# Kernel tuning notes

Hardware: AMD Instinct MI355X
Metric: run time of the kernel (lower is better)

The kernel has to match this reference:

```python
import jax, jax.numpy as jnp
import numpy as np

B_SCENES = 2; K = 5; C = 128; H = 64; W = 64
D_INNER = C; D_STATE = 16; DT_RANK = 8
C_TUKEY = 0.3; ALPHA = 2.0; BETA = 0.4; GAMMA = 0.8


def affine_grid(theta, Ho, Wo):
    # torch F.affine_grid, align_corners=False (pixel centers)
    xs = (jnp.arange(Wo, dtype=jnp.float32) + 0.5) * (2.0 / Wo) - 1.0
    ys = (jnp.arange(Ho, dtype=jnp.float32) + 0.5) * (2.0 / Ho) - 1.0
    gx, gy = jnp.meshgrid(xs, ys)
    base = jnp.stack([gx, gy, jnp.ones_like(gx)], axis=-1)  # (H,W,3)
    return jnp.einsum('nij,hwj->nhwi', theta, base)  # (N,H,W,2)


def grid_sample(src, grid):
    # bilinear, zero padding, align_corners=False; src (N,C,H,W), grid (N,H,W,2)
    N, Cc, Hs, Ws = src.shape
    ix = ((grid[..., 0] + 1.0) * Ws - 1.0) * 0.5
    iy = ((grid[..., 1] + 1.0) * Hs - 1.0) * 0.5
    x0 = jnp.floor(ix); y0 = jnp.floor(iy)
    def tap(xf, yf):
        v = ((xf >= 0) & (xf <= Ws - 1) & (yf >= 0) & (yf <= Hs - 1)).astype(src.dtype)
        xc = jnp.clip(xf, 0, Ws - 1).astype(jnp.int32)
        yc = jnp.clip(yf, 0, Hs - 1).astype(jnp.int32)
        vals = jax.vmap(lambda s, y, x: s[:, y, x])(src, yc, xc)  # (N,C,H,W)
        return vals * v[:, None]
    wx1 = (ix - x0)[:, None]; wy1 = (iy - y0)[:, None]
    wx0 = 1.0 - wx1; wy0 = 1.0 - wy1
    return (tap(x0, y0) * wx0 * wy0 + tap(x0 + 1.0, y0) * wx1 * wy0
            + tap(x0, y0 + 1.0) * wx0 * wy1 + tap(x0 + 1.0, y0 + 1.0) * wx1 * wy1)


def ss2d(tokens, in_proj_w, conv_w, conv_b, x_proj_w, dt_w, dt_b, A_logs, Ds, ln_g, ln_b, out_proj_w):
    # tokens (C, Hs, Ws) channel-first; VMamba-style v05_noz core, d_inner=C
    xin = jnp.einsum('chw,dc->dhw', tokens, in_proj_w)
    xc = jax.lax.conv_general_dilated(xin[None], conv_w, (1, 1), [(1, 1), (1, 1)],
                                      dimension_numbers=('NCHW', 'OIHW', 'NCHW'),
                                      feature_group_count=D_INNER)[0] + conv_b[:, None, None]
    xa = jax.nn.silu(xc)
    d, Hs, Ws = xa.shape
    L = Hs * Ws
    x_hw = xa.reshape(d, L)
    x_wh = jnp.swapaxes(xa, 1, 2).reshape(d, L)
    xs = jnp.stack([x_hw, x_wh, x_hw[:, ::-1], x_wh[:, ::-1]], axis=0)  # (4,d,L)
    x_dbl = jnp.einsum('kdl,kcd->kcl', xs, x_proj_w)
    dt = x_dbl[:, :DT_RANK]
    Bm = x_dbl[:, DT_RANK:DT_RANK + D_STATE]
    Cm = x_dbl[:, DT_RANK + D_STATE:]
    dts = jax.nn.softplus(jnp.einsum('kdr,krl->kdl', dt_w, dt) + dt_b[..., None])
    A = -jnp.exp(A_logs)  # (4,d,n)
    seq = (jnp.moveaxis(xs, -1, 0), jnp.moveaxis(dts, -1, 0),
           jnp.moveaxis(Bm, -1, 0), jnp.moveaxis(Cm, -1, 0))
    def step(h, inp):
        xt, dtt, Bt, Ct = inp
        h = h * jnp.exp(dtt[..., None] * A) + (dtt * xt)[..., None] * Bt[:, None, :]
        return h, jnp.einsum('kdn,kn->kd', h, Ct)
    h0 = jnp.zeros((4, d, D_STATE), tokens.dtype)
    _, ys = jax.lax.scan(jax.checkpoint(step), h0, seq)  # ys (L,4,d)
    ys = jnp.moveaxis(ys, 0, -1) + Ds[..., None] * xs  # (4,d,L)
    untr = lambda y: jnp.swapaxes(y.reshape(d, Ws, Hs), 1, 2).reshape(d, L)
    y = ys[0] + untr(ys[1]) + ys[2][:, ::-1] + untr(ys[3][:, ::-1])
    yt = y.T  # (L,d)
    mu = yt.mean(-1, keepdims=True)
    var = ((yt - mu) ** 2).mean(-1, keepdims=True)
    yn = (yt - mu) * jax.lax.rsqrt(var + 1e-5) * ln_g + ln_b
    out = yn @ out_proj_w.T  # (L,C)
    return jnp.moveaxis(out.reshape(Hs, Ws, -1), -1, 0)  # (C,Hs,Ws)


def forward(x, nam, in_proj_w, conv_w, conv_b, x_proj_w, dt_w, dt_b, A_logs, Ds, ln_g, ln_b, out_proj_w):
    xg = x.reshape(B_SCENES, K, C, H, W)  # record_len is constant K
    t_rows = nam[:, 0]  # ego row i=0 of t_matrix: (B,K,2,3)
    def scene(xb, t_row):
        warped = grid_sample(xb, affine_grid(t_row, H, W))  # (K,C,H,W)
        ego = warped[0]
        # per-pixel cosine sim across channels (F.normalize(dim=0) on (C,HW) views)
        en = ego / jnp.maximum(jnp.sqrt((ego ** 2).sum(0, keepdims=True)), 1e-6)
        nb = warped / jnp.maximum(jnp.sqrt((warped ** 2).sum(1, keepdims=True)), 1e-6)
        sims = jnp.clip((en[None] * nb).sum(1), -1.0, 1.0)  # (K,H,W)
        r = jnp.maximum(1.0 - sims, 0.0)
        xr = jnp.maximum(r / C_TUKEY, 0.0)
        w_pix = jnp.maximum(jnp.maximum(1.0 - xr * xr, 0.0) ** 2, 1e-6)[:, None]  # (K,1,H,W)
        tx = t_row[:, 0, 2]; ty = t_row[:, 1, 2]
        yaw = jnp.abs(jnp.arctan2(t_row[:, 0, 1], t_row[:, 0, 0]))
        g = jax.nn.sigmoid(ALPHA - BETA * jnp.sqrt(tx ** 2 + ty ** 2) - GAMMA * yaw)  # (K,)
        logit = jnp.log(w_pix + 1e-8) + jnp.log(g + 1e-8)[:, None, None, None]
        alpha = jax.nn.softmax(logit, axis=0)  # softmax over K per pixel
        weighted = warped * alpha
        tokens = jnp.swapaxes(weighted.reshape(K, C, H * W), 0, 1)  # (C,K,HW)
        out = ss2d(tokens, in_proj_w, conv_w, conv_b, x_proj_w, dt_w, dt_b,
                   A_logs, Ds, ln_g, ln_b, out_proj_w)  # (C,K,HW)
        return jnp.swapaxes(out, 0, 1).reshape(K, C, W, H)[0]  # (C,W,H) as in original view
    return jax.vmap(scene)(xg, t_rows)


def setup_inputs() -> dict:
    key = jax.random.key(0)
    ks = jax.random.split(key, 10)
    x = jax.random.normal(ks[0], (B_SCENES * K, C, H, W), jnp.float32)
    record_len = jnp.full((B_SCENES,), K, dtype=jnp.int32)
    eye = jnp.broadcast_to(jnp.array([[1.0, 0.0, 0.0], [0.0, 1.0, 0.0]], jnp.float32),
                           (B_SCENES, K, K, 2, 3))
    nam = eye + 0.05 * jax.random.normal(ks[1], (B_SCENES, K, K, 2, 3), jnp.float32)
    in_proj_w = 0.05 * jax.random.normal(ks[2], (D_INNER, C), jnp.float32)
    conv_w = 0.1 * jax.random.normal(ks[3], (D_INNER, 1, 3, 3), jnp.float32)
    conv_b = jnp.zeros((D_INNER,), jnp.float32)
    x_proj_w = 0.05 * jax.random.normal(ks[4], (4, DT_RANK + 2 * D_STATE, D_INNER), jnp.float32)
    dt_w = 0.1 * jax.random.normal(ks[5], (4, D_INNER, DT_RANK), jnp.float32)
    dt_b = -4.6 + 0.5 * jax.random.normal(ks[6], (4, D_INNER), jnp.float32)
    A_logs = jnp.broadcast_to(jnp.log(jnp.arange(1, D_STATE + 1, dtype=jnp.float32)),
                              (4, D_INNER, D_STATE)) + jnp.zeros((4, D_INNER, D_STATE), jnp.float32)
    Ds = jnp.ones((4, D_INNER), jnp.float32)
    ln_g = jnp.ones((D_INNER,), jnp.float32)
    ln_b = jnp.zeros((D_INNER,), jnp.float32)
    out_proj_w = 0.05 * jax.random.normal(ks[7], (C, D_INNER), jnp.float32)
    return {"x": x, "record_len": record_len, "normalized_affine_matrix": nam,
            "in_proj_w": in_proj_w, "conv_w": conv_w, "conv_b": conv_b,
            "x_proj_w": x_proj_w, "dt_w": dt_w, "dt_b": dt_b, "A_logs": A_logs,
            "Ds": Ds, "ln_g": ln_g, "ln_b": ln_b, "out_proj_w": out_proj_w}


def reference(x, record_len, normalized_affine_matrix, in_proj_w, conv_w, conv_b,
              x_proj_w, dt_w, dt_b, A_logs, Ds, ln_g, ln_b, out_proj_w):
    # record_len is a constant (= K per scene) and only determines the static grouping
    return forward(x, normalized_affine_matrix, in_proj_w, conv_w, conv_b,
                   x_proj_w, dt_w, dt_b, A_logs, Ds, ln_g, ln_b, out_proj_w)
```

## Files before the change

kernel.cpp:

```cpp
#include <hip/hip_runtime.h>
#include <math.h>

#define B_S   2
#define PIX   4096
#define LL    20480
#define NS    16
#define RR    8
#define NCHK  512
#define LC    40
#define SUBS  10
#define NSUB  4
#define NGRP  32
#define GCH   16
#define K0CH  104

typedef float v2f __attribute__((ext_vector_type(2)));
typedef float v4f __attribute__((ext_vector_type(4)));

__device__ __forceinline__ v2f pk_mul(v2f a, v2f b) {
  v2f d;
  asm("v_pk_mul_f32 %0, %1, %2" : "=v"(d) : "v"(a), "v"(b));
  return d;
}
#define PK_FMA_ACC(a, b, c) asm("v_pk_fma_f32 %0, %1, %2, %0" : "+v"(a) : "v"(b), "v"(c))
#define PK_DECAY(h, e, m) asm("v_pk_fma_f32 %0, %0, %1, %2" : "+v"(h) : "v"(e), "v"(m))

template<int K>
__device__ __forceinline__ int zmapT(int l) {
  if (K == 0) return l;
  if (K == 1) return ((l % 5) << 12) + l / 5;
  if (K == 2) return 20479 - l;
  int lr = 20479 - l;
  return ((lr % 5) << 12) + lr / 5;
}

__global__ __launch_bounds__(256)
void k_warp(const float* __restrict__ x, const float* __restrict__ nam,
            float* __restrict__ warped) {
  __shared__ float wL[4][64];
  __shared__ int   iL[4][64];
  int blk = blockIdx.x;
  int bk = blk >> 11;
  int rem = blk & 2047;
  int ct = rem >> 6, pt = rem & 63;
  int p0 = pt * 64;
  int t = threadIdx.x;
  int pl = t & 63, cg = t >> 6;
  if (t < 64) {
    int b = bk / 5, k = bk - b * 5;
    const float* th = nam + (size_t)(b * 25 + k) * 6;
    int p = p0 + t;
    float gx = ((p & 63) + 0.5f) * 0.03125f - 1.0f;
    float gy = ((p >> 6) + 0.5f) * 0.03125f - 1.0f;
    float grx = th[0] * gx + th[1] * gy + th[2];
    float gry = th[3] * gx + th[4] * gy + th[5];
    float ix = ((grx + 1.0f) * 64.0f - 1.0f) * 0.5f;
    float iy = ((gry + 1.0f) * 64.0f - 1.0f) * 0.5f;
    float x0 = floorf(ix), y0 = floorf(iy);
    float fx = ix - x0, fy = iy - y0;
    float vx0 = (x0 >= 0.0f && x0 <= 63.0f) ? 1.0f : 0.0f;
    float vx1 = (x0 >= -1.0f && x0 <= 62.0f) ? 1.0f : 0.0f;
    float vy0 = (y0 >= 0.0f && y0 <= 63.0f) ? 1.0f : 0.0f;
    float vy1 = (y0 >= -1.0f && y0 <= 62.0f) ? 1.0f : 0.0f;
    int xi0 = (int)fminf(fmaxf(x0, 0.0f), 63.0f);
    int yi0 = (int)fminf(fmaxf(y0, 0.0f), 63.0f);
    int xi1 = (int)fminf(fmaxf(x0 + 1.0f, 0.0f), 63.0f);
    int yi1 = (int)fminf(fmaxf(y0 + 1.0f, 0.0f), 63.0f);
    wL[0][t] = (1.0f - fx) * (1.0f - fy) * vx0 * vy0;
    wL[1][t] = fx * (1.0f - fy) * vx1 * vy0;
    wL[2][t] = (1.0f - fx) * fy * vx0 * vy1;
    wL[3][t] = fx * fy * vx1 * vy1;
    iL[0][t] = yi0 * 64 + xi0;
    iL[1][t] = yi0 * 64 + xi1;
    iL[2][t] = yi1 * 64 + xi0;
    iL[3][t] = yi1 * 64 + xi1;
  }
  __syncthreads();
  int c = ct * 4 + cg;
  const float* src = x + (size_t)(bk * 128 + c) * PIX;
  float acc = wL[0][pl] * src[iL[0][pl]]
            + wL[1][pl] * src[iL[1][pl]]
            + wL[2][pl] * src[iL[2][pl]]
            + wL[3][pl] * src[iL[3][pl]];
  warped[((size_t)(bk * 128 + c)) * PIX + p0 + pl] = acc;
}

__global__ __launch_bounds__(512)
void k_alpha(const float* __restrict__ warped, const float* __restrict__ nam,
             float* __restrict__ alpha) {
  __shared__ float part[8][64][9];
  int blk = blockIdx.x;
  int b = blk >> 6;
  int p0 = (blk & 63) << 6;
  int wv = threadIdx.x >> 6, lane = threadIdx.x & 63;
  int p = p0 + lane;
  const float* wb = warped + (size_t)b * 5 * 128 * PIX + p;
  float dot[5] = {0,0,0,0,0}, ssq[5] = {0,0,0,0,0};
  int c0 = wv * 16;
  for (int c = c0; c < c0 + 16; ++c) {
    float w0 = wb[(size_t)c * PIX];
    ssq[0] += w0 * w0;
    #pragma unroll
    for (int k = 1; k < 5; ++k) {
      float wk = wb[((size_t)k * 128 + c) * PIX];
      dot[k] += w0 * wk;
      ssq[k] += wk * wk;
    }
  }
  part[wv][lane][0] = ssq[0];
  #pragma unroll
  for (int k = 1; k < 5; ++k) {
    part[wv][lane][k] = dot[k];
    part[wv][lane][4 + k] = ssq[k];
  }
  __syncthreads();
  if (threadIdx.x < 64) {
    float q[9];
    #pragma unroll
    for (int j = 0; j < 9; ++j) {
      float s = 0.0f;
      #pragma unroll
      for (int w = 0; w < 8; ++w) s += part[w][lane][j];
      q[j] = s;
    }
    float n0 = fmaxf(sqrtf(q[0]), 1e-6f);
    float logit[5];
    #pragma unroll
    for (int k = 0; k < 5; ++k) {
      float dotk = (k == 0) ? q[0] : q[k];
      float ssqk = (k == 0) ? q[0] : q[4 + k];
      float nk = fmaxf(sqrtf(ssqk), 1e-6f);
      float sim = fminf(fmaxf(dotk / (n0 * nk), -1.0f), 1.0f);
      float r = fmaxf(1.0f - sim, 0.0f);
      float xr = r * (1.0f / 0.3f);
      float tt = fmaxf(1.0f - xr * xr, 0.0f);
      float wp = fmaxf(tt * tt, 1e-6f);
      const float* th = nam + (size_t)(b * 25 + k) * 6;
      float tx = th[2], ty = th[5];
      float yaw = fabsf(atan2f(th[1], th[0]));
      float gk = 1.0f / (1.0f + __expf(-(2.0f - 0.4f * sqrtf(tx*tx + ty*ty) - 0.8f * yaw)));
      logit[k] = __logf(wp + 1e-8f) + __logf(gk + 1e-8f);
    }
    float m = logit[0];
    #pragma unroll
    for (int k = 1; k < 5; ++k) m = fmaxf(m, logit[k]);
    float e[5], s = 0.0f;
    #pragma unroll
    for (int k = 0; k < 5; ++k) { e[k] = __expf(logit[k] - m); s += e[k]; }
    float inv = 1.0f / s;
    #pragma unroll
    for (int k = 0; k < 5; ++k)
      alpha[((size_t)(b * 5 + k)) * PIX + p] = e[k] * inv;
  }
}

__global__ __launch_bounds__(256, 4)
void k_gemm_in(const float* __restrict__ warped, const float* __restrict__ alpha,
               const float* __restrict__ W, float* __restrict__ X0) {
  __shared__ float xl[64][129];
  __shared__ __align__(16) float wlT[32][132];
  int t = threadIdx.x;
  int row0 = blockIdx.x * 64;
  int b = row0 / LL;
  int z0 = row0 - b * LL;
  int a = z0 >> 12;
  int p0 = z0 & 4095;
  int ba = b * 5 + a;
  int r = t & 63, cg = t >> 6;
  float av = alpha[(size_t)ba * PIX + p0 + r];
  #pragma unroll
  for (int i = 0; i < 32; ++i) {
    int c = cg * 32 + i;
    xl[r][c] = warped[((size_t)ba * 128 + c) * PIX + p0 + r] * av;
  }
  int zl2 = t & 31;
  int mg  = t >> 5;
  float acc0[16], acc1[16];
  #pragma unroll
  for (int i = 0; i < 16; ++i) { acc0[i] = 0.0f; acc1[i] = 0.0f; }
  for (int c0 = 0; c0 < 128; c0 += 32) {
    __syncthreads();
    #pragma unroll
    for (int i = 0; i < 16; ++i) {
      int m = (t >> 5) * 16 + i;
      wlT[t & 31][m] = W[(size_t)m * 128 + c0 + (t & 31)];
    }
    __syncthreads();
    const float* xr0 = xl[2 * zl2];
    const float* xr1 = xl[2 * zl2 + 1];
    for (int cc = 0; cc < 32; ++cc) {
      float xv0 = xr0[c0 + cc];
      float xv1 = xr1[c0 + cc];
      const float4* wr = (const float4*)(&wlT[cc][mg * 16]);
      #pragma unroll
      for (int q = 0; q < 4; ++q) {
        float4 w4 = wr[q];
        acc0[q*4+0] = fmaf(w4.x, xv0, acc0[q*4+0]);
        acc0[q*4+1] = fmaf(w4.y, xv0, acc0[q*4+1]);
        acc0[q*4+2] = fmaf(w4.z, xv0, acc0[q*4+2]);
        acc0[q*4+3] = fmaf(w4.w, xv0, acc0[q*4+3]);
        acc1[q*4+0] = fmaf(w4.x, xv1, acc1[q*4+0]);
        acc1[q*4+1] = fmaf(w4.y, xv1, acc1[q*4+1]);
        acc1[q*4+2] = fmaf(w4.z, xv1, acc1[q*4+2]);
        acc1[q*4+3] = fmaf(w4.w, xv1, acc1[q*4+3]);
      }
    }
  }
  __syncthreads();
  #pragma unroll
  for (int q = 0; q < 16; ++q) {
    xl[2 * zl2][mg * 16 + q] = acc0[q];
    xl[2 * zl2 + 1][mg * 16 + q] = acc1[q];
  }
  __syncthreads();
  #pragma unroll
  for (int i = 0; i < 32; ++i) {
    int idx = i * 256 + t;
    X0[((size_t)row0 + (idx >> 7)) * 128 + (idx & 127)] = xl[idx >> 7][idx & 127];
  }
}

__global__ __launch_bounds__(256)
void k_conv(const float* __restrict__ X0, const float* __restrict__ cw,
            const float* __restrict__ cb, float* __restrict__ XT) {
  int g = blockIdx.x * 256 + threadIdx.x;
  int d = g & 127;
  int zz4 = g >> 7;
  int b = zz4 / (LL / 4);
  int r = zz4 - b * (LL / 4);
  int z0 = r * 4;
  int a = z0 >> 12, p = z0 & 4095;
  float w9[9];
  #pragma unroll
  for (int i = 0; i < 9; ++i) w9[i] = cw[d * 9 + i];
  float cbv = cb[d];
  float acc[4] = {cbv, cbv, cbv, cbv};
  #pragma unroll
  for (int di = 0; di < 3; ++di) {
    int aa = a + di - 1;
    if (aa < 0 || aa >= 5) continue;
    const float* rowb = X0 + ((size_t)b * LL + (size_t)aa * PIX) * 128 + d;
    #pragma unroll
    for (int dj = -1; dj <= 4; ++dj) {
      int pp = p + dj;
      if (pp < 0 || pp >= PIX) continue;
      float v = rowb[(size_t)pp * 128];
      #pragma unroll
      for (int o = 0; o < 4; ++o) {
        int rel = dj - o;
        if (rel >= -1 && rel <= 1) acc[o] = fmaf(w9[di * 3 + rel + 1], v, acc[o]);
      }
    }
  }
  float* dst = XT + (size_t)(zz4 * 4) * 128 + d;
  #pragma unroll
  for (int o = 0; o < 4; ++o) {
    float sg = 1.0f / (1.0f + __expf(-acc[o]));
    dst[(size_t)o * 128] = acc[o] * sg;
  }
}

__global__ __launch_bounds__(256, 4)
void k_gemmZ(const float* __restrict__ X, const float* __restrict__ W,
             float* __restrict__ ZdtB, float* __restrict__ ZC) {
  __shared__ float xl[64][129];
  __shared__ __align__(16) float wlT[32][164];
  int t = threadIdx.x;
  int row0 = blockIdx.x * 64;
  #pragma unroll
  for (int i = 0; i < 32; ++i) {
    int idx = i * 256 + t;
    xl[idx >> 7][idx & 127] = X[((size_t)row0 + (idx >> 7)) * 128 + (idx & 127)];
  }
  int zl2 = t & 31;
  int mg  = t >> 5;
  float acc0[20], acc1[20];
  #pragma unroll
  for (int i = 0; i < 20; ++i) { acc0[i] = 0.0f; acc1[i] = 0.0f; }
  for (int c0 = 0; c0 < 128; c0 += 32) {
    __syncthreads();
    #pragma unroll
    for (int i = 0; i < 20; ++i) {
      int m = (t >> 5) * 20 + i;
      wlT[t & 31][m] = W[(size_t)m * 128 + c0 + (t & 31)];
    }
    __syncthreads();
    const float* xr0 = xl[2 * zl2];
    const float* xr1 = xl[2 * zl2 + 1];
    for (int cc = 0; cc < 32; ++cc) {
      float xv0 = xr0[c0 + cc];
      float xv1 = xr1[c0 + cc];
      const float4* wr = (const float4*)(&wlT[cc][mg * 20]);
      #pragma unroll
      for (int q = 0; q < 5; ++q) {
        float4 w4 = wr[q];
        acc0[q*4+0] = fmaf(w4.x, xv0, acc0[q*4+0]);
        acc0[q*4+1] = fmaf(w4.y, xv0, acc0[q*4+1]);
        acc0[q*4+2] = fmaf(w4.z, xv0, acc0[q*4+2]);
        acc0[q*4+3] = fmaf(w4.w, xv0, acc0[q*4+3]);
        acc1[q*4+0] = fmaf(w4.x, xv1, acc1[q*4+0]);
        acc1[q*4+1] = fmaf(w4.y, xv1, acc1[q*4+1]);
        acc1[q*4+2] = fmaf(w4.z, xv1, acc1[q*4+2]);
        acc1[q*4+3] = fmaf(w4.w, xv1, acc1[q*4+3]);
      }
    }
  }
  int dir = mg >> 1;
  int halfc = mg & 1;
  #pragma unroll
  for (int rr = 0; rr < 2; ++rr) {
    const float* acc = rr ? acc1 : acc0;
    int row = row0 + 2 * zl2 + rr;
    int b = row / LL, z = row - b * LL;
    int a = z >> 12, qq = z & 4095;
    int l;
    if (dir == 0)      l = z;
    else if (dir == 1) l = 5 * qq + a;
    else if (dir == 2) l = 20479 - z;
    else               l = 20479 - (5 * qq + a);
    size_t seqrow = (size_t)(b * 4 + dir) * LL + l;
    if (halfc == 0) {
      float* dD = ZdtB + seqrow * 24;
      #pragma unroll
      for (int q2 = 0; q2 < 5; ++q2)
        *(float4*)(dD + q2 * 4) = make_float4(acc[q2*4], acc[q2*4+1], acc[q2*4+2], acc[q2*4+3]);
    } else {
      float* dD = ZdtB + seqrow * 24;
      *(float4*)(dD + 20) = make_float4(acc[0], acc[1], acc[2], acc[3]);
      float* dC = ZC + seqrow * 16;
      #pragma unroll
      for (int q2 = 0; q2 < 4; ++q2)
        *(float4*)(dC + q2 * 4) = make_float4(acc[4+q2*4], acc[4+q2*4+1], acc[4+q2*4+2], acc[4+q2*4+3]);
    }
  }
}

template<int K>
__device__ void scan_body(int b, int chunk, int dh, int lane,
    const float* __restrict__ XT, const float* __restrict__ ZdtB,
    const float* __restrict__ ZC,
    const float* __restrict__ dt_w, const float* __restrict__ dt_b,
    const float* __restrict__ A_logs, const float* __restrict__ Ds,
    const int* __restrict__ chainflags,
    float* __restrict__ h_out, float* __restrict__ sumdts,
    float* __restrict__ ysz, float* __restrict__ cumqv,
    float* stD, float* stC)
{
  const int d = dh * 64 + lane;
  const int kd = K * 128 + d;
  bool chainok = chainflags[kd] != 0;
  float dw[8];
  #pragma unroll
  for (int r = 0; r < 8; ++r) dw[r] = dt_w[(size_t)kd * 8 + r];
  const float dtb = dt_b[kd], dsv = Ds[kd];
  v2f h2[8];
  #pragma unroll
  for (int n = 0; n < 8; ++n) h2[n] = (v2f){0.0f, 0.0f};
  float sdt = 0.0f;
  float qrun = 1.0f;
  const int seq = b * 4 + K;
  const float* ZDs = ZdtB + (size_t)seq * LL * 24;
  const float* ZCs = ZC + (size_t)seq * LL * 16;
  const float* Xb = XT + (size_t)b * LL * 128;
  float* ysb = ysz + (size_t)seq * PIX * 128;
  float* cqb = cumqv + (size_t)seq * PIX * 128;
  const int l0 = chunk * LC;

  if (__all(chainok ? 1 : 0)) {
    #pragma unroll 1
    for (int sub = 0; sub < NSUB; ++sub) {
      const int ls = l0 + sub * SUBS;
      {
        const v4f* srcD = (const v4f*)(ZDs + (size_t)ls * 24);
        if (lane < SUBS * 6) ((v4f*)stD)[lane] = srcD[lane];
      }
      int s0c = 0;
      bool needC;
      if (K == 0)      needC = (ls < PIX);
      else if (K == 2) needC = (ls + SUBS > LL - PIX);
      else             needC = true;
      if (K == 1) s0c = (5 - (ls % 5)) % 5;
      if (K == 3) s0c = (9 - (ls % 5)) % 5;
      if (needC) {
        if (K == 0 || K == 2) {
          const v4f* srcC = (const v4f*)(ZCs + (size_t)ls * 16);
          if (lane < SUBS * 4) ((v4f*)stC)[lane] = srcC[lane];
        } else {
          if (lane < 8) {
            int l = ls + s0c + 5 * (lane >> 2);
            if (l > LL - 1) l = LL - 1;
            ((v4f*)stC)[lane] = *(const v4f*)(ZCs + (size_t)l * 16 + (lane & 3) * 4);
          }
        }
      }
      float xr[SUBS];
      #pragma unroll
      for (int s = 0; s < SUBS; ++s) {
        int z = zmapT<K>(ls + s);
        xr[s] = Xb[(size_t)z * 128 + d];
      }
      int zc = 0;
      if (K == 1) zc = (ls + s0c) / 5;
      if (K == 3) zc = (20479 - ls - s0c) / 5;
      int yj = 0;
      #pragma unroll
      for (int s = 0; s < SUBS; ++s) {
        const v4f* rowD4 = (const v4f*)(stD + s * 24);
        v4f rA = rowD4[0], rB = rowD4[1];
        float dtl = dtb;
        dtl = fmaf(dw[0], rA[0], dtl); dtl = fmaf(dw[1], rA[1], dtl);
        dtl = fmaf(dw[2], rA[2], dtl); dtl = fmaf(dw[3], rA[3], dtl);
        dtl = fmaf(dw[4], rB[0], dtl); dtl = fmaf(dw[5], rB[1], dtl);
        dtl = fmaf(dw[6], rB[2], dtl); dtl = fmaf(dw[7], rB[3], dtl);
        float edt = __expf(dtl);
        float e1 = __builtin_amdgcn_rcpf(1.0f + edt);
        float dt = (dtl > 20.0f) ? dtl : __logf(1.0f + edt);
        sdt += dt;
        qrun *= e1;
        float xsv = xr[s];
        float dtx = dt * xsv;
        v2f dtx2 = {dtx, dtx};
        float e2 = e1 * e1;
        v2f E[8];
        E[0] = (v2f){e1, e2};
        v2f e2s = {e2, e2};
        E[1] = pk_mul(E[0], e2s);
        E[2] = pk_mul(E[1], e2s);
        E[3] = pk_mul(E[2], e2s);
        float e8 = E[3][1];
        v2f e8s = {e8, e8};
        E[4] = pk_mul(E[0], e8s);
        E[5] = pk_mul(E[1], e8s);
        E[6] = pk_mul(E[2], e8s);
        E[7] = pk_mul(E[3], e8s);
        v4f B0 = rowD4[2], B1 = rowD4[3], B2v = rowD4[4], B3 = rowD4[5];
        v2f m;
        m = pk_mul(dtx2, (v2f){B0[0], B0[1]});  PK_DECAY(h2[0], E[0], m);
        m = pk_mul(dtx2, (v2f){B0[2], B0[3]});  PK_DECAY(h2[1], E[1], m);
        m = pk_mul(dtx2, (v2f){B1[0], B1[1]});  PK_DECAY(h2[2], E[2], m);
        m = pk_mul(dtx2, (v2f){B1[2], B1[3]});  PK_DECAY(h2[3], E[3], m);
        m = pk_mul(dtx2, (v2f){B2v[0], B2v[1]}); PK_DECAY(h2[4], E[4], m);
        m = pk_mul(dtx2, (v2f){B2v[2], B2v[3]}); PK_DECAY(h2[5], E[5], m);
        m = pk_mul(dtx2, (v2f){B3[0], B3[1]});  PK_DECAY(h2[6], E[6], m);
        m = pk_mul(dtx2, (v2f){B3[2], B3[3]});  PK_DECAY(h2[7], E[7], m);
        bool doY;
        int z;
        if (K == 0)      { z = ls + s;            doY = (z < PIX); }
        else if (K == 2) { z = 20479 - (ls + s);  doY = (z < PIX); }
        else             { z = zc;                doY = ((s % 5) == s0c); }
        if (doY) {
          const v4f* C4 = (const v4f*)(stC + ((K == 0 || K == 2) ? s : yj) * 16);
          v4f C0 = C4[0], C1 = C4[1], C2v = C4[2], C3 = C4[3];
          v2f ya = pk_mul(h2[0], (v2f){C0[0], C0[1]});
          PK_FMA_ACC(ya, h2[1], ((v2f){C0[2], C0[3]}));
          PK_FMA_ACC(ya, h2[2], ((v2f){C1[0], C1[1]}));
          PK_FMA_ACC(ya, h2[3], ((v2f){C1[2], C1[3]}));
          PK_FMA_ACC(ya, h2[4], ((v2f){C2v[0], C2v[1]}));
          PK_FMA_ACC(ya, h2[5], ((v2f){C2v[2], C2v[3]}));
          PK_FMA_ACC(ya, h2[6], ((v2f){C3[0], C3[1]}));
          PK_FMA_ACC(ya, h2[7], ((v2f){C3[2], C3[3]}));
          float y = fmaf(dsv, xsv, ya[0] + ya[1]);
          size_t o = (size_t)z * 128 + d;
          ysb[o] = y;
          cqb[o] = qrun;
          ++yj;
          if (K == 1) ++zc;
          if (K == 3) --zc;
        }
      }
    }
  } else {
    float An[NS];
    #pragma unroll
    for (int n = 0; n < NS; ++n) An[n] = -__expf(A_logs[(size_t)kd * 16 + n]);
    float hs[NS];
    #pragma unroll
    for (int n = 0; n < NS; ++n) hs[n] = 0.0f;
    #pragma unroll 1
    for (int l = l0; l < l0 + LC; ++l) {
      int z = zmapT<K>(l);
      const float* rowD = ZDs + (size_t)l * 24;
      float dtl = dtb;
      #pragma unroll
      for (int r = 0; r < RR; ++r) dtl += dw[r] * rowD[r];
      float edt = __expf(dtl);
      float dt = (dtl > 20.0f) ? dtl : __logf(1.0f + edt);
      sdt += dt;
      float xv = Xb[(size_t)z * 128 + d];
      float dtx = dt * xv;
      #pragma unroll
      for (int n = 0; n < NS; ++n)
        hs[n] = hs[n] * __expf(dt * An[n]) + dtx * rowD[8 + n];
      if (z < PIX) {
        const float* rowC = ZCs + (size_t)l * 16;
        float y = dsv * xv;
        #pragma unroll
        for (int n = 0; n < NS; ++n) y = fmaf(hs[n], rowC[n], y);
        size_t o = (size_t)z * 128 + d;
        ysb[o] = y;
        cqb[o] = __expf(-sdt);
      }
    }
    #pragma unroll
    for (int n = 0; n < 8; ++n) h2[n] = (v2f){hs[2*n], hs[2*n+1]};
  }
  float* ho = h_out + (((size_t)seq * NCHK + chunk) * 128 + d) * 16;
  #pragma unroll
  for (int n = 0; n < 8; ++n) {
    ho[2*n] = h2[n][0];
    ho[2*n+1] = h2[n][1];
  }
  sumdts[((size_t)seq * NCHK + chunk) * 128 + d] = sdt;
}

__global__ __launch_bounds__(128, 8)
void k_scan1(const float* __restrict__ XT, const float* __restrict__ ZdtB,
             const float* __restrict__ ZC,
             const float* __restrict__ dt_w, const float* __restrict__ dt_b,
             const float* __restrict__ A_logs, const float* __restrict__ Ds,
             const int* __restrict__ chainflags,
             float* __restrict__ h_out, float* __restrict__ sumdts,
             float* __restrict__ ysz, float* __restrict__ cumqv) {
  __shared__ __align__(16) float stD_all[2][SUBS * 24];
  __shared__ __align__(16) float stC_all[2][SUBS * 16];
  int tid = threadIdx.x, wid = tid >> 6, lane = tid & 63;
  int bid = blockIdx.x;
  int bb = bid / (K0CH + 3 * NCHK);
  int idx = bid - bb * (K0CH + 3 * NCHK);
  int k, chunk;
  if (idx < K0CH)                 { k = 0; chunk = idx; }
  else if (idx < K0CH + NCHK)     { k = 1; chunk = idx - K0CH; }
  else if (idx < K0CH + 2 * NCHK) { k = 2; chunk = idx - (K0CH + NCHK); }
  else                            { k = 3; chunk = idx - (K0CH + 2 * NCHK); }
  int dh = wid;
  float* stD = stD_all[wid];
  float* stC = stC_all[wid];
  switch (k) {
    case 0: scan_body<0>(bb, chunk, dh, lane, XT, ZdtB, ZC, dt_w, dt_b, A_logs, Ds, chainflags, h_out, sumdts, ysz, cumqv, stD, stC); break;
    case 1: scan_body<1>(bb, chunk, dh, lane, XT, ZdtB, ZC, dt_w, dt_b, A_logs, Ds, chainflags, h_out, sumdts, ysz, cumqv, stD, stC); break;
    case 2: scan_body<2>(bb, chunk, dh, lane, XT, ZdtB, ZC, dt_w, dt_b, A_logs, Ds, chainflags, h_out, sumdts, ysz, cumqv, stD, stC); break;
    default: scan_body<3>(bb, chunk, dh, lane, XT, ZdtB, ZC, dt_w, dt_b, A_logs, Ds, chainflags, h_out, sumdts, ysz, cumqv, stD, stC); break;
  }
}

__global__ __launch_bounds__(256)
void k_comb_a(const float* __restrict__ A_logs, const float* __restrict__ sumdts,
              const float* __restrict__ h_out, float* __restrict__ Ag,
              float* __restrict__ Bg) {
  int g = blockIdx.x * 256 + threadIdx.x;
  int n = g & 15;
  int d = (g >> 4) & 127;
  int grp = (g >> 11) & 31;
  int seq = g >> 16;
  int k = seq & 3;
  if (k == 0 && grp > 6) return;
  float An = -__expf(A_logs[(size_t)(k * 128 + d) * 16 + n]);
  float A = 1.0f, Bv = 0.0f;
  size_t cbase = (size_t)seq * NCHK + grp * GCH;
  #pragma unroll 4
  for (int j = 0; j < GCH; ++j) {
    float a = __expf(An * sumdts[(cbase + j) * 128 + d]);
    float b = h_out[((cbase + j) * 128 + d) * 16 + n];
    A *= a;
    Bv = Bv * a + b;
  }
  size_t o = (((size_t)seq * NGRP + grp) * 128 + d) * 16 + n;
  Ag[o] = A;
  Bg[o] = Bv;
}

__global__ __launch_bounds__(256)
void k_comb_b(const float* __restrict__ Ag, const float* __restrict__ Bg,
              float* __restrict__ Hg) {
  int g = blockIdx.x * 256 + threadIdx.x;
  int n = g & 15;
  int d = (g >> 4) & 127;
  int seq = g >> 11;
  float H = 0.0f;
  #pragma unroll
  for (int grp = 0; grp < NGRP; ++grp) {
    size_t o = (((size_t)seq * NGRP + grp) * 128 + d) * 16 + n;
    Hg[o] = H;
    H = Ag[o] * H + Bg[o];
  }
}

__global__ __launch_bounds__(256)
void k_comb_c(const float* __restrict__ A_logs, const float* __restrict__ sumdts,
              const float* __restrict__ h_out, const float* __restrict__ Hg,
              float* __restrict__ h_in) {
  int g = blockIdx.x * 256 + threadIdx.x;
  int n = g & 15;
  int d = (g >> 4) & 127;
  int grp = (g >> 11) & 31;
  int seq = g >> 16;
  int k = seq & 3;
  if (k == 0 && grp > 6) return;
  if (k == 2 && grp < 25) return;
  float An = -__expf(A_logs[(size_t)(k * 128 + d) * 16 + n]);
  float h = Hg[(((size_t)seq * NGRP + grp) * 128 + d) * 16 + n];
  size_t cbase = (size_t)seq * NCHK + grp * GCH;
  #pragma unroll 4
  for (int j = 0; j < GCH; ++j) {
    size_t o = ((cbase + j) * 128 + d) * 16 + n;
    h_in[o] = h;
    float a = __expf(An * sumdts[(cbase + j) * 128 + d]);
    h = a * h + h_out[o];
  }
}

__global__ __launch_bounds__(256)
void k_wt(const float* __restrict__ Wo, float* __restrict__ WT,
          const float* __restrict__ A_logs, int* __restrict__ chainflags) {
  if (blockIdx.x >= 16) {
    int kd = (blockIdx.x - 16) * 256 + threadIdx.x;
    bool c = true;
    #pragma unroll
    for (int n = 0; n < NS; ++n) {
      float An = -__expf(A_logs[(size_t)kd * 16 + n]);
      c = c && (fabsf(An + (float)(n + 1)) < 3e-5f * (float)(n + 1));
    }
    chainflags[kd] = c ? 1 : 0;
    return;
  }
  __shared__ float tl[32][33];
  int bx = blockIdx.x & 3, by = blockIdx.x >> 2;
  int t = threadIdx.x;
  int tx = t & 31, ty = t >> 5;
  #pragma unroll
  for (int i = 0; i < 4; ++i)
    tl[ty + i * 8][tx] = Wo[(size_t)(by * 32 + ty + i * 8) * 128 + bx * 32 + tx];
  __syncthreads();
  #pragma unroll
  for (int i = 0; i < 4; ++i)
    WT[(size_t)(bx * 32 + ty + i * 8) * 128 + by * 32 + tx] = tl[tx][ty + i * 8];
}

__global__ __launch_bounds__(256)
void k_merge(const float* __restrict__ ysz, const float* __restrict__ ZC,
             const float* __restrict__ A_logs, const float* __restrict__ h_in,
             const float* __restrict__ cumq, const int* __restrict__ chainflags,
             const float* __restrict__ ln_g, const float* __restrict__ ln_b,
             const float* __restrict__ WT, float* __restrict__ out) {
  __shared__ __align__(16) float ynT[128][20];
  __shared__ float red[4][8][2];
  int blk = blockIdx.x;
  int b = blk >> 8;
  int p0 = (blk & 255) * 16;
  int tid = threadIdx.x;
  int t = tid & 127;
  int half = tid >> 7;
  int w = tid >> 6;
  float g = ln_g[t], bb = ln_b[t];
  bool cok[4];
  #pragma unroll
  for (int k = 0; k < 4; ++k) cok[k] = chainflags[k * 128 + t] != 0;
  float yv[8];
  #pragma unroll
  for (int i = 0; i < 8; ++i) {
    int p = p0 + 2 * i + half;
    float y = 0.0f;
    #pragma unroll
    for (int k = 0; k < 4; ++k) {
      size_t zi = ((size_t)(b * 4 + k) * PIX + p) * 128 + t;
      float yk = ysz[zi];
      int l;
      if (k == 0)      l = p;
      else if (k == 1) l = 5 * p;
      else if (k == 2) l = 20479 - p;
      else             l = 20479 - 5 * p;
      int chunk = l / LC;
      float q = cumq[zi];
      const v2f* hi2 = (const v2f*)(h_in + (((size_t)(b * 4 + k) * NCHK + chunk) * 128 + t) * 16);
      const v2f* Cr2 = (const v2f*)(ZC + ((size_t)(b * 4 + k) * LL + l) * 16);
      float fix;
      if (cok[k]) {
        float q2 = q * q;
        v2f Q[8];
        Q[0] = (v2f){q, q2};
        v2f q2s = {q2, q2};
        Q[1] = pk_mul(Q[0], q2s);
        Q[2] = pk_mul(Q[1], q2s);
        Q[3] = pk_mul(Q[2], q2s);
        float q8 = Q[3][1];
        v2f q8s = {q8, q8};
        Q[4] = pk_mul(Q[0], q8s);
        Q[5] = pk_mul(Q[1], q8s);
        Q[6] = pk_mul(Q[2], q8s);
        Q[7] = pk_mul(Q[3], q8s);
        v2f a = pk_mul(pk_mul(hi2[0], Cr2[0]), Q[0]);
        #pragma unroll
        for (int j = 1; j < 8; ++j) {
          v2f m = pk_mul(hi2[j], Cr2[j]);
          PK_FMA_ACC(a, m, Q[j]);
        }
        fix = a[0] + a[1];
      } else {
        float cd = -__logf(q);
        fix = 0.0f;
        const float* hi = (const float*)hi2;
        const float* Cr = (const float*)Cr2;
        #pragma unroll
        for (int n = 0; n < NS; ++n) {
          float An = -__expf(A_logs[(size_t)(k * 128 + t) * 16 + n]);
          fix += Cr[n] * hi[n] * __expf(An * cd);
        }
      }
      y += yk + fix;
    }
    yv[i] = y;
    float s1 = y, s2 = y * y;
    #pragma unroll
    for (int off = 32; off; off >>= 1) {
      s1 += __shfl_xor(s1, off);
      s2 += __shfl_xor(s2, off);
    }
    if ((tid & 63) == 0) { red[w][i][0] = s1; red[w][i][1] = s2; }
  }
  __syncthreads();
  #pragma unroll
  for (int i = 0; i < 8; ++i) {
    int pl = 2 * i + half;
    float S1 = red[half * 2][i][0] + red[half * 2 + 1][i][0];
    float S2 = red[half * 2][i][1] + red[half * 2 + 1][i][1];
    float mu = S1 * (1.0f / 128.0f);
    float var = S2 * (1.0f / 128.0f) - mu * mu;
    float rs = rsqrtf(var + 1e-5f);
    ynT[t][pl] = (yv[i] - mu) * rs * g + bb;
  }
  __syncthreads();
  float acc[8];
  #pragma unroll
  for (int i = 0; i < 8; ++i) acc[i] = 0.0f;
  for (int dd = 0; dd < 128; ++dd) {
    float wv = WT[(size_t)dd * 128 + t];
    const float4* yr = (const float4*)(&ynT[dd][half * 8]);
    float4 ya = yr[0], yb4 = yr[1];
    acc[0] = fmaf(ya.x,  wv, acc[0]);
    acc[1] = fmaf(ya.y,  wv, acc[1]);
    acc[2] = fmaf(ya.z,  wv, acc[2]);
    acc[3] = fmaf(ya.w,  wv, acc[3]);
    acc[4] = fmaf(yb4.x, wv, acc[4]);
    acc[5] = fmaf(yb4.y, wv, acc[5]);
    acc[6] = fmaf(yb4.z, wv, acc[6]);
    acc[7] = fmaf(yb4.w, wv, acc[7]);
  }
  float* dst = out + ((size_t)b * 128 + t) * PIX + p0 + half * 8;
  *(float4*)(dst)     = make_float4(acc[0], acc[1], acc[2], acc[3]);
  *(float4*)(dst + 4) = make_float4(acc[4], acc[5], acc[6], acc[7]);
}

extern "C" void kernel_launch(void* const* d_in, const int* in_sizes, int n_in,
                              void* d_out, int out_size, void* d_ws, size_t ws_size,
                              hipStream_t stream) {
  const float* x         = (const float*)d_in[0];
  const float* nam       = (const float*)d_in[2];
  const float* in_proj_w = (const float*)d_in[3];
  const float* conv_w    = (const float*)d_in[4];
  const float* conv_b    = (const float*)d_in[5];
  const float* x_proj_w  = (const float*)d_in[6];
  const float* dt_w      = (const float*)d_in[7];
  const float* dt_b      = (const float*)d_in[8];
  const float* A_logs    = (const float*)d_in[9];
  const float* Ds        = (const float*)d_in[10];
  const float* ln_g      = (const float*)d_in[11];
  const float* ln_b      = (const float*)d_in[12];
  const float* out_proj_w= (const float*)d_in[13];
  float* out = (float*)d_out;
  float* ws  = (float*)d_ws;

  float* warped = ws;
  float* alpha  = warped + 5242880;
  float* X0     = alpha  + 40960;
  float* XT     = X0     + 5242880;
  float* ZdtB   = XT     + 5242880;
  float* ZC     = ZdtB   + 3932160;
  float* sums   = ZC     + 2621440;
  float* ysz    = sums   + 524288;
  float* cumq   = ysz    + 4194304;
  float* WT     = cumq   + 4194304;
  float* Ag     = WT     + 16384;
  float* Bg     = Ag     + 524288;
  float* Hg     = Bg     + 524288;
  int*   chainflags = (int*)(Hg + 524288);

  float* h_out = ws;
  float* h_in  = XT;

  k_wt     <<<18,    256, 0, stream>>>(out_proj_w, WT, A_logs, chainflags);
  k_warp   <<<20480, 256, 0, stream>>>(x, nam, warped);
  k_alpha  <<<128,   512, 0, stream>>>(warped, nam, alpha);
  k_gemm_in<<<640,   256, 0, stream>>>(warped, alpha, in_proj_w, X0);
  k_conv   <<<5120,  256, 0, stream>>>(X0, conv_w, conv_b, XT);
  k_gemmZ  <<<640,   256, 0, stream>>>(XT, x_proj_w, ZdtB, ZC);
  k_scan1  <<<B_S * (K0CH + 3 * NCHK), 128, 0, stream>>>(XT, ZdtB, ZC, dt_w, dt_b,
                                                         A_logs, Ds, chainflags,
                                                         h_out, sums, ysz, cumq);
  k_comb_a <<<2048,  256, 0, stream>>>(A_logs, sums, h_out, Ag, Bg);
  k_comb_b <<<64,    256, 0, stream>>>(Ag, Bg, Hg);
  k_comb_c <<<2048,  256, 0, stream>>>(A_logs, sums, h_out, Hg, h_in);
  k_merge  <<<512,   256, 0, stream>>>(ysz, ZC, A_logs, h_in, cumq, chainflags,
                                       ln_g, ln_b, WT, out);
}
```

Measured before the change: 245.3 us.

## Interleave two independent scan chunks per thread to hide recurrence latency

Each scan thread now processes two adjacent 40-step chunks, interleaving their per-step updates so the two independent recurrences can overlap in the instruction pipeline. The grid is halved and launch bounds drop from 8 to 4 waves per SIMD to make room for the doubled state registers. Shared staging buffers are doubled per wave. The cost is fewer resident waves and fewer blocks, which may reduce latency hiding for memory loads.

```diff
diff --git a/kernel.cpp b/kernel.cpp
--- a/kernel.cpp
+++ b/kernel.cpp
@@ -12,7 +12,7 @@
 #define NSUB  4
 #define NGRP  32
 #define GCH   16
-#define K0CH  104
+#define K0CP  52
 
 typedef float v2f __attribute__((ext_vector_type(2)));
 typedef float v4f __attribute__((ext_vector_type(4)));
@@ -335,8 +335,62 @@
   }
 }
 
+#define STEP1(H, SDT, QRUN, STD, STC, XV, ZVAL, DOY, CIDX)                    \
+  {                                                                           \
+    const v4f* rowD4_ = (const v4f*)((STD) + s * 24);                         \
+    v4f rA_ = rowD4_[0], rB_ = rowD4_[1];                                     \
+    float dtl_ = dtb;                                                         \
+    dtl_ = fmaf(dw[0], rA_[0], dtl_); dtl_ = fmaf(dw[1], rA_[1], dtl_);       \
+    dtl_ = fmaf(dw[2], rA_[2], dtl_); dtl_ = fmaf(dw[3], rA_[3], dtl_);       \
+    dtl_ = fmaf(dw[4], rB_[0], dtl_); dtl_ = fmaf(dw[5], rB_[1], dtl_);       \
+    dtl_ = fmaf(dw[6], rB_[2], dtl_); dtl_ = fmaf(dw[7], rB_[3], dtl_);       \
+    float edt_ = __expf(dtl_);                                                \
+    float e1_ = __builtin_amdgcn_rcpf(1.0f + edt_);                           \
+    float dt_ = (dtl_ > 20.0f) ? dtl_ : __logf(1.0f + edt_);                  \
+    SDT += dt_; QRUN *= e1_;                                                  \
+    float dtx_ = dt_ * (XV);                                                  \
+    v2f dtx2_ = {dtx_, dtx_};                                                 \
+    float e2_ = e1_ * e1_;                                                    \
+    v2f E0_ = (v2f){e1_, e2_};                                                \
+    v2f e2s_ = {e2_, e2_};                                                    \
+    v2f E1_ = pk_mul(E0_, e2s_);                                              \
+    v2f E2_ = pk_mul(E1_, e2s_);                                              \
+    v2f E3_ = pk_mul(E2_, e2s_);                                              \
+    float e8_ = E3_[1];                                                       \
+    v2f e8s_ = {e8_, e8_};                                                    \
+    v2f E4_ = pk_mul(E0_, e8s_);                                              \
+    v2f E5_ = pk_mul(E1_, e8s_);                                              \
+    v2f E6_ = pk_mul(E2_, e8s_);                                              \
+    v2f E7_ = pk_mul(E3_, e8s_);                                              \
+    v4f B0_ = rowD4_[2], B1_ = rowD4_[3], B2_ = rowD4_[4], B3_ = rowD4_[5];   \
+    v2f m_;                                                                   \
+    m_ = pk_mul(dtx2_, (v2f){B0_[0], B0_[1]});  PK_DECAY(H[0], E0_, m_);      \
+    m_ = pk_mul(dtx2_, (v2f){B0_[2], B0_[3]});  PK_DECAY(H[1], E1_, m_);      \
+    m_ = pk_mul(dtx2_, (v2f){B1_[0], B1_[1]});  PK_DECAY(H[2], E2_, m_);      \
+    m_ = pk_mul(dtx2_, (v2f){B1_[2], B1_[3]});  PK_DECAY(H[3], E3_, m_);      \
+    m_ = pk_mul(dtx2_, (v2f){B2_[0], B2_[1]});  PK_DECAY(H[4], E4_, m_);      \
+    m_ = pk_mul(dtx2_, (v2f){B2_[2], B2_[3]});  PK_DECAY(H[5], E5_, m_);      \
+    m_ = pk_mul(dtx2_, (v2f){B3_[0], B3_[1]});  PK_DECAY(H[6], E6_, m_);      \
+    m_ = pk_mul(dtx2_, (v2f){B3_[2], B3_[3]});  PK_DECAY(H[7], E7_, m_);      \
+    if (DOY) {                                                                \
+      const v4f* C4_ = (const v4f*)((STC) + (CIDX) * 16);                     \
+      v4f C0_ = C4_[0], C1_ = C4_[1], C2_ = C4_[2], C3_ = C4_[3];             \
+      v2f ya_ = pk_mul(H[0], (v2f){C0_[0], C0_[1]});                          \
+      PK_FMA_ACC(ya_, H[1], ((v2f){C0_[2], C0_[3]}));                         \
+      PK_FMA_ACC(ya_, H[2], ((v2f){C1_[0], C1_[1]}));                         \
+      PK_FMA_ACC(ya_, H[3], ((v2f){C1_[2], C1_[3]}));                         \
+      PK_FMA_ACC(ya_, H[4], ((v2f){C2_[0], C2_[1]}));                         \
+      PK_FMA_ACC(ya_, H[5], ((v2f){C2_[2], C2_[3]}));                         \
+      PK_FMA_ACC(ya_, H[6], ((v2f){C3_[0], C3_[1]}));                         \
+      PK_FMA_ACC(ya_, H[7], ((v2f){C3_[2], C3_[3]}));                         \
+      float y_ = fmaf(dsv, (XV), ya_[0] + ya_[1]);                            \
+      size_t o_ = (size_t)(ZVAL) * 128 + d;                                   \
+      ysb[o_] = y_; cqb[o_] = QRUN;                                           \
+    }                                                                         \
+  }
+
 template<int K>
-__device__ void scan_body(int b, int chunk, int dh, int lane,
+__device__ void scan_body(int b, int c0, int dh, int lane,
     const float* __restrict__ XT, const float* __restrict__ ZdtB,
     const float* __restrict__ ZC,
     const float* __restrict__ dt_w, const float* __restrict__ dt_b,
@@ -344,7 +398,7 @@
     const int* __restrict__ chainflags,
     float* __restrict__ h_out, float* __restrict__ sumdts,
     float* __restrict__ ysz, float* __restrict__ cumqv,
-    float* stD, float* stC)
+    float* stDA, float* stDB, float* stCA, float* stCB)
 {
   const int d = dh * 64 + lane;
   const int kd = K * 128 + d;
@@ -353,167 +407,140 @@
   #pragma unroll
   for (int r = 0; r < 8; ++r) dw[r] = dt_w[(size_t)kd * 8 + r];
   const float dtb = dt_b[kd], dsv = Ds[kd];
-  v2f h2[8];
-  #pragma unroll
-  for (int n = 0; n < 8; ++n) h2[n] = (v2f){0.0f, 0.0f};
-  float sdt = 0.0f;
-  float qrun = 1.0f;
+  v2f h2a[8], h2b[8];
+  #pragma unroll
+  for (int n = 0; n < 8; ++n) { h2a[n] = (v2f){0.0f, 0.0f}; h2b[n] = (v2f){0.0f, 0.0f}; }
+  float sdtA = 0.0f, sdtB = 0.0f, qA = 1.0f, qB = 1.0f;
   const int seq = b * 4 + K;
   const float* ZDs = ZdtB + (size_t)seq * LL * 24;
   const float* ZCs = ZC + (size_t)seq * LL * 16;
   const float* Xb = XT + (size_t)b * LL * 128;
   float* ysb = ysz + (size_t)seq * PIX * 128;
   float* cqb = cumqv + (size_t)seq * PIX * 128;
-  const int l0 = chunk * LC;
+  const int lA0 = c0 * LC;
 
   if (__all(chainok ? 1 : 0)) {
     #pragma unroll 1
     for (int sub = 0; sub < NSUB; ++sub) {
-      const int ls = l0 + sub * SUBS;
+      const int lsA = lA0 + sub * SUBS;
+      const int lsB = lsA + LC;
       {
-        const v4f* srcD = (const v4f*)(ZDs + (size_t)ls * 24);
-        if (lane < SUBS * 6) ((v4f*)stD)[lane] = srcD[lane];
-      }
-      int s0c = 0;
-      bool needC;
-      if (K == 0)      needC = (ls < PIX);
-      else if (K == 2) needC = (ls + SUBS > LL - PIX);
-      else             needC = true;
-      if (K == 1) s0c = (5 - (ls % 5)) % 5;
-      if (K == 3) s0c = (9 - (ls % 5)) % 5;
-      if (needC) {
-        if (K == 0 || K == 2) {
-          const v4f* srcC = (const v4f*)(ZCs + (size_t)ls * 16);
-          if (lane < SUBS * 4) ((v4f*)stC)[lane] = srcC[lane];
-        } else {
-          if (lane < 8) {
-            int l = ls + s0c + 5 * (lane >> 2);
-            if (l > LL - 1) l = LL - 1;
-            ((v4f*)stC)[lane] = *(const v4f*)(ZCs + (size_t)l * 16 + (lane & 3) * 4);
-          }
+        const v4f* sA = (const v4f*)(ZDs + (size_t)lsA * 24);
+        const v4f* sB = (const v4f*)(ZDs + (size_t)lsB * 24);
+        if (lane < SUBS * 6) {
+          ((v4f*)stDA)[lane] = sA[lane];
+          ((v4f*)stDB)[lane] = sB[lane];
         }
       }
-      float xr[SUBS];
+      int s0cA = 0, s0cB = 0;
+      if (K == 1) { s0cA = (5 - (lsA % 5)) % 5; s0cB = (5 - (lsB % 5)) % 5; }
+      if (K == 3) { s0cA = (9 - (lsA % 5)) % 5; s0cB = (9 - (lsB % 5)) % 5; }
+      if (K == 0 || K == 2) {
+        bool nCA = (K == 0) ? (lsA < PIX) : (lsA + SUBS > LL - PIX);
+        bool nCB = (K == 0) ? (lsB < PIX) : (lsB + SUBS > LL - PIX);
+        if (nCA && lane < SUBS * 4)
+          ((v4f*)stCA)[lane] = ((const v4f*)(ZCs + (size_t)lsA * 16))[lane];
+        if (nCB && lane < SUBS * 4)
+          ((v4f*)stCB)[lane] = ((const v4f*)(ZCs + (size_t)lsB * 16))[lane];
+      } else {
+        if (lane < 8) {
+          int l = lsA + s0cA + 5 * (lane >> 2);
+          if (l > LL - 1) l = LL - 1;
+          ((v4f*)stCA)[lane] = *(const v4f*)(ZCs + (size_t)l * 16 + (lane & 3) * 4);
+        } else if (lane < 16) {
+          int ll = lane - 8;
+          int l = lsB + s0cB + 5 * (ll >> 2);
+          if (l > LL - 1) l = LL - 1;
+          ((v4f*)stCB)[ll] = *(const v4f*)(ZCs + (size_t)l * 16 + (ll & 3) * 4);
+        }
+      }
+      float xrA[SUBS], xrB[SUBS];
       #pragma unroll
       for (int s = 0; s < SUBS; ++s) {
-        int z = zmapT<K>(ls + s);
-        xr[s] = Xb[(size_t)z * 128 + d];
-      }
-      int zc = 0;
-      if (K == 1) zc = (ls + s0c) / 5;
-      if (K == 3) zc = (20479 - ls - s0c) / 5;
-      int yj = 0;
+        xrA[s] = Xb[(size_t)zmapT<K>(lsA + s) * 128 + d];
+        xrB[s] = Xb[(size_t)zmapT<K>(lsB + s) * 128 + d];
+      }
+      int zcA = 0, zcB = 0;
+      if (K == 1) { zcA = (lsA + s0cA) / 5; zcB = (lsB + s0cB) / 5; }
+      if (K == 3) { zcA = (20479 - lsA - s0cA) / 5; zcB = (20479 - lsB - s0cB) / 5; }
+      int yjA = 0, yjB = 0;
       #pragma unroll
       for (int s = 0; s < SUBS; ++s) {
-        const v4f* rowD4 = (const v4f*)(stD + s * 24);
-        v4f rA = rowD4[0], rB = rowD4[1];
+        bool doYA; int zA;
+        if (K == 0)      { zA = lsA + s;            doYA = (zA < PIX); }
+        else if (K == 2) { zA = 20479 - (lsA + s);  doYA = (zA < PIX); }
+        else             { zA = zcA;                doYA = ((s % 5) == s0cA); }
+        int ciA = (K == 0 || K == 2) ? s : yjA;
+        STEP1(h2a, sdtA, qA, stDA, stCA, xrA[s], zA, doYA, ciA);
+        if (doYA) { ++yjA; if (K == 1) ++zcA; if (K == 3) --zcA; }
+        bool doYB; int zB;
+        if (K == 0)      { zB = lsB + s;            doYB = (zB < PIX); }
+        else if (K == 2) { zB = 20479 - (lsB + s);  doYB = (zB < PIX); }
+        else             { zB = zcB;                doYB = ((s % 5) == s0cB); }
+        int ciB = (K == 0 || K == 2) ? s : yjB;
+        STEP1(h2b, sdtB, qB, stDB, stCB, xrB[s], zB, doYB, ciB);
+        if (doYB) { ++yjB; if (K == 1) ++zcB; if (K == 3) --zcB; }
+      }
+    }
+  } else {
+    float An[NS];
+    #pragma unroll
+    for (int n = 0; n < NS; ++n) An[n] = -__expf(A_logs[(size_t)kd * 16 + n]);
+    #pragma unroll 1
+    for (int half = 0; half < 2; ++half) {
+      float hs[NS];
+      #pragma unroll
+      for (int n = 0; n < NS; ++n) hs[n] = 0.0f;
+      float sdt = 0.0f;
+      int l0 = (c0 + half) * LC;
+      #pragma unroll 1
+      for (int l = l0; l < l0 + LC; ++l) {
+        int z = zmapT<K>(l);
+        const float* rowD = ZDs + (size_t)l * 24;
         float dtl = dtb;
-        dtl = fmaf(dw[0], rA[0], dtl); dtl = fmaf(dw[1], rA[1], dtl);
-        dtl = fmaf(dw[2], rA[2], dtl); dtl = fmaf(dw[3], rA[3], dtl);
-        dtl = fmaf(dw[4], rB[0], dtl); dtl = fmaf(dw[5], rB[1], dtl);
-        dtl = fmaf(dw[6], rB[2], dtl); dtl = fmaf(dw[7], rB[3], dtl);
+        #pragma unroll
+        for (int r = 0; r < RR; ++r) dtl += dw[r] * rowD[r];
         float edt = __expf(dtl);
-        float e1 = __builtin_amdgcn_rcpf(1.0f + edt);
         float dt = (dtl > 20.0f) ? dtl : __logf(1.0f + edt);
         sdt += dt;
-        qrun *= e1;
-        float xsv = xr[s];
-        float dtx = dt * xsv;
-        v2f dtx2 = {dtx, dtx};
-        float e2 = e1 * e1;
-        v2f E[8];
-        E[0] = (v2f){e1, e2};
-        v2f e2s = {e2, e2};
-        E[1] = pk_mul(E[0], e2s);
-        E[2] = pk_mul(E[1], e2s);
-        E[3] = pk_mul(E[2], e2s);
-        float e8 = E[3][1];
-        v2f e8s = {e8, e8};
-        E[4] = pk_mul(E[0], e8s);
-        E[5] = pk_mul(E[1], e8s);
-        E[6] = pk_mul(E[2], e8s);
-        E[7] = pk_mul(E[3], e8s);
-        v4f B0 = rowD4[2], B1 = rowD4[3], B2v = rowD4[4], B3 = rowD4[5];
-        v2f m;
-        m = pk_mul(dtx2, (v2f){B0[0], B0[1]});  PK_DECAY(h2[0], E[0], m);
-        m = pk_mul(dtx2, (v2f){B0[2], B0[3]});  PK_DECAY(h2[1], E[1], m);
-        m = pk_mul(dtx2, (v2f){B1[0], B1[1]});  PK_DECAY(h2[2], E[2], m);
-        m = pk_mul(dtx2, (v2f){B1[2], B1[3]});  PK_DECAY(h2[3], E[3], m);
-        m = pk_mul(dtx2, (v2f){B2v[0], B2v[1]}); PK_DECAY(h2[4], E[4], m);
-        m = pk_mul(dtx2, (v2f){B2v[2], B2v[3]}); PK_DECAY(h2[5], E[5], m);
-        m = pk_mul(dtx2, (v2f){B3[0], B3[1]});  PK_DECAY(h2[6], E[6], m);
-        m = pk_mul(dtx2, (v2f){B3[2], B3[3]});  PK_DECAY(h2[7], E[7], m);
-        bool doY;
-        int z;
-        if (K == 0)      { z = ls + s;            doY = (z < PIX); }
-        else if (K == 2) { z = 20479 - (ls + s);  doY = (z < PIX); }
-        else             { z = zc;                doY = ((s % 5) == s0c); }
-        if (doY) {
-          const v4f* C4 = (const v4f*)(stC + ((K == 0 || K == 2) ? s : yj) * 16);
-          v4f C0 = C4[0], C1 = C4[1], C2v = C4[2], C3 = C4[3];
-          v2f ya = pk_mul(h2[0], (v2f){C0[0], C0[1]});
-          PK_FMA_ACC(ya, h2[1], ((v2f){C0[2], C0[3]}));
-          PK_FMA_ACC(ya, h2[2], ((v2f){C1[0], C1[1]}));
-          PK_FMA_ACC(ya, h2[3], ((v2f){C1[2], C1[3]}));
-          PK_FMA_ACC(ya, h2[4], ((v2f){C2v[0], C2v[1]}));
-          PK_FMA_ACC(ya, h2[5], ((v2f){C2v[2], C2v[3]}));
-          PK_FMA_ACC(ya, h2[6], ((v2f){C3[0], C3[1]}));
-          PK_FMA_ACC(ya, h2[7], ((v2f){C3[2], C3[3]}));
-          float y = fmaf(dsv, xsv, ya[0] + ya[1]);
+        float xv = Xb[(size_t)z * 128 + d];
+        float dtx = dt * xv;
+        #pragma unroll
+        for (int n = 0; n < NS; ++n)
+          hs[n] = hs[n] * __expf(dt * An[n]) + dtx * rowD[8 + n];
+        if (z < PIX) {
+          const float* rowC = ZCs + (size_t)l * 16;
+          float y = dsv * xv;
+          #pragma unroll
+          for (int n = 0; n < NS; ++n) y = fmaf(hs[n], rowC[n], y);
           size_t o = (size_t)z * 128 + d;
           ysb[o] = y;
-          cqb[o] = qrun;
-          ++yj;
-          if (K == 1) ++zc;
-          if (K == 3) --zc;
+          cqb[o] = __expf(-sdt);
         }
       }
-    }
-  } else {
-    float An[NS];
-    #pragma unroll
-    for (int n = 0; n < NS; ++n) An[n] = -__expf(A_logs[(size_t)kd * 16 + n]);
-    float hs[NS];
-    #pragma unroll
-    for (int n = 0; n < NS; ++n) hs[n] = 0.0f;
-    #pragma unroll 1
-    for (int l = l0; l < l0 + LC; ++l) {
-      int z = zmapT<K>(l);
-      const float* rowD = ZDs + (size_t)l * 24;
-      float dtl = dtb;
-      #pragma unroll
-      for (int r = 0; r < RR; ++r) dtl += dw[r] * rowD[r];
-      float edt = __expf(dtl);
-      float dt = (dtl > 20.0f) ? dtl : __logf(1.0f + edt);
-      sdt += dt;
-      float xv = Xb[(size_t)z * 128 + d];
-      float dtx = dt * xv;
-      #pragma unroll
-      for (int n = 0; n < NS; ++n)
-        hs[n] = hs[n] * __expf(dt * An[n]) + dtx * rowD[8 + n];
-      if (z < PIX) {
-        const float* rowC = ZCs + (size_t)l * 16;
-        float y = dsv * xv;
+      if (half == 0) {
+        sdtA = sdt;
         #pragma unroll
-        for (int n = 0; n < NS; ++n) y = fmaf(hs[n], rowC[n], y);
-        size_t o = (size_t)z * 128 + d;
-        ysb[o] = y;
-        cqb[o] = __expf(-sdt);
-      }
-    }
-    #pragma unroll
-    for (int n = 0; n < 8; ++n) h2[n] = (v2f){hs[2*n], hs[2*n+1]};
-  }
-  float* ho = h_out + (((size_t)seq * NCHK + chunk) * 128 + d) * 16;
+        for (int n = 0; n < 8; ++n) h2a[n] = (v2f){hs[2*n], hs[2*n+1]};
+      } else {
+        sdtB = sdt;
+        #pragma unroll
+        for (int n = 0; n < 8; ++n) h2b[n] = (v2f){hs[2*n], hs[2*n+1]};
+      }
+    }
+  }
+  float* hoA = h_out + (((size_t)seq * NCHK + c0) * 128 + d) * 16;
+  float* hoB = h_out + (((size_t)seq * NCHK + c0 + 1) * 128 + d) * 16;
   #pragma unroll
   for (int n = 0; n < 8; ++n) {
-    ho[2*n] = h2[n][0];
-    ho[2*n+1] = h2[n][1];
-  }
-  sumdts[((size_t)seq * NCHK + chunk) * 128 + d] = sdt;
-}
-
-__global__ __launch_bounds__(128, 8)
+    hoA[2*n] = h2a[n][0]; hoA[2*n+1] = h2a[n][1];
+    hoB[2*n] = h2b[n][0]; hoB[2*n+1] = h2b[n][1];
+  }
+  sumdts[((size_t)seq * NCHK + c0) * 128 + d] = sdtA;
+  sumdts[((size_t)seq * NCHK + c0 + 1) * 128 + d] = sdtB;
+}
+
+__global__ __launch_bounds__(128, 4)
 void k_scan1(const float* __restrict__ XT, const float* __restrict__ ZdtB,
              const float* __restrict__ ZC,
              const float* __restrict__ dt_w, const float* __restrict__ dt_b,
@@ -521,25 +548,28 @@
              const int* __restrict__ chainflags,
              float* __restrict__ h_out, float* __restrict__ sumdts,
              float* __restrict__ ysz, float* __restrict__ cumqv) {
-  __shared__ __align__(16) float stD_all[2][SUBS * 24];
-  __shared__ __align__(16) float stC_all[2][SUBS * 16];
+  __shared__ __align__(16) float stD_all[2][2][SUBS * 24];
+  __shared__ __align__(16) float stC_all[2][2][SUBS * 16];
   int tid = threadIdx.x, wid = tid >> 6, lane = tid & 63;
   int bid = blockIdx.x;
-  int bb = bid / (K0CH + 3 * NCHK);
-  int idx = bid - bb * (K0CH + 3 * NCHK);
-  int k, chunk;
-  if (idx < K0CH)                 { k = 0; chunk = idx; }
-  else if (idx < K0CH + NCHK)     { k = 1; chunk = idx - K0CH; }
-  else if (idx < K0CH + 2 * NCHK) { k = 2; chunk = idx - (K0CH + NCHK); }
-  else                            { k = 3; chunk = idx - (K0CH + 2 * NCHK); }
+  int bb = bid / (K0CP + 768);
+  int idx = bid - bb * (K0CP + 768);
+  int k, cpair;
+  if (idx < K0CP)            { k = 0; cpair = idx; }
+  else if (idx < K0CP + 256) { k = 1; cpair = idx - K0CP; }
+  else if (idx < K0CP + 512) { k = 2; cpair = idx - (K0CP + 256); }
+  else                       { k = 3; cpair = idx - (K0CP + 512); }
+  int c0 = cpair * 2;
   int dh = wid;
-  float* stD = stD_all[wid];
-  float* stC = stC_all[wid];
+  float* stDA = stD_all[wid][0];
+  float* stDB = stD_all[wid][1];
+  float* stCA = stC_all[wid][0];
+  float* stCB = stC_all[wid][1];
   switch (k) {
-    case 0: scan_body<0>(bb, chunk, dh, lane, XT, ZdtB, ZC, dt_w, dt_b, A_logs, Ds, chainflags, h_out, sumdts, ysz, cumqv, stD, stC); break;
-    case 1: scan_body<1>(bb, chunk, dh, lane, XT, ZdtB, ZC, dt_w, dt_b, A_logs, Ds, chainflags, h_out, sumdts, ysz, cumqv, stD, stC); break;
-    case 2: scan_body<2>(bb, chunk, dh, lane, XT, ZdtB, ZC, dt_w, dt_b, A_logs, Ds, chainflags, h_out, sumdts, ysz, cumqv, stD, stC); break;
-    default: scan_body<3>(bb, chunk, dh, lane, XT, ZdtB, ZC, dt_w, dt_b, A_logs, Ds, chainflags, h_out, sumdts, ysz, cumqv, stD, stC); break;
+    case 0: scan_body<0>(bb, c0, dh, lane, XT, ZdtB, ZC, dt_w, dt_b, A_logs, Ds, chainflags, h_out, sumdts, ysz, cumqv, stDA, stDB, stCA, stCB); break;
+    case 1: scan_body<1>(bb, c0, dh, lane, XT, ZdtB, ZC, dt_w, dt_b, A_logs, Ds, chainflags, h_out, sumdts, ysz, cumqv, stDA, stDB, stCA, stCB); break;
+    case 2: scan_body<2>(bb, c0, dh, lane, XT, ZdtB, ZC, dt_w, dt_b, A_logs, Ds, chainflags, h_out, sumdts, ysz, cumqv, stDA, stDB, stCA, stCB); break;
+    default: scan_body<3>(bb, c0, dh, lane, XT, ZdtB, ZC, dt_w, dt_b, A_logs, Ds, chainflags, h_out, sumdts, ysz, cumqv, stDA, stDB, stCA, stCB); break;
   }
 }
 
@@ -793,9 +823,9 @@
   k_gemm_in<<<640,   256, 0, stream>>>(warped, alpha, in_proj_w, X0);
   k_conv   <<<5120,  256, 0, stream>>>(X0, conv_w, conv_b, XT);
   k_gemmZ  <<<640,   256, 0, stream>>>(XT, x_proj_w, ZdtB, ZC);
-  k_scan1  <<<B_S * (K0CH + 3 * NCHK), 128, 0, stream>>>(XT, ZdtB, ZC, dt_w, dt_b,
-                                                         A_logs, Ds, chainflags,
-                                                         h_out, sums, ysz, cumq);
+  k_scan1  <<<B_S * (K0CP + 768), 128, 0, stream>>>(XT, ZdtB, ZC, dt_w, dt_b,
+                                                    A_logs, Ds, chainflags,
+                                                    h_out, sums, ysz, cumq);
   k_comb_a <<<2048,  256, 0, stream>>>(A_logs, sums, h_out, Ag, Bg);
   k_comb_b <<<64,    256, 0, stream>>>(Ag, Bg, Hg);
   k_comb_c <<<2048,  256, 0, stream>>>(A_logs, sums, h_out, Hg, h_in);
```

Result: slower. 251.8 us (+2.7%).
